# Kernel optimization log

Hardware: AMD Instinct MI355X
Metric: run time of the kernel (lower is better)

Reference implementation:

```python
import jax, jax.numpy as jnp
import numpy as np

B, R, IMG_DIM, TAG_DIM = 256, 36, 2048, 768
BOX_LEN = 15
POS_EMBED = 200
POS_SIZE = 16 * 16 + 1  # 257
EMBED_SIZE = 1024
EPS_NORM = 1e-8
EPS_ATTN = 1e-6


def setup_inputs() -> dict:
    key = jax.random.key(0)
    ks = jax.random.split(key, 8)
    images = jax.random.normal(ks[0], (B, R, IMG_DIM), dtype=jnp.float32)
    images_tag = jax.random.normal(ks[1], (B, R, TAG_DIM), dtype=jnp.float32)
    # boxes: first 15 entries are integer position indices, last 15 are weights
    box_idx = jax.random.randint(ks[2], (B, R, BOX_LEN), 0, POS_SIZE).astype(jnp.float32)
    box_w = jax.random.uniform(ks[3], (B, R, BOX_LEN), dtype=jnp.float32)
    boxes = jnp.concatenate([box_idx, box_w], axis=-1)  # [B,R,30]
    # parameters (xavier-uniform-like for linears, normal for embedding)
    pos_emb = jax.random.normal(ks[4], (POS_SIZE, POS_EMBED), dtype=jnp.float32)
    fan = (IMG_DIM + TAG_DIM) + POS_EMBED
    r1 = np.sqrt(6.0) / np.sqrt(fan)
    attn_W = jax.random.uniform(ks[5], (POS_EMBED, IMG_DIM + TAG_DIM), dtype=jnp.float32, minval=-r1, maxval=r1)
    fc_in = IMG_DIM + POS_EMBED + TAG_DIM
    r2 = np.sqrt(6.0) / np.sqrt(fc_in + EMBED_SIZE)
    fc_W = jax.random.uniform(ks[6], (EMBED_SIZE, fc_in), dtype=jnp.float32, minval=-r2, maxval=r2)
    fc_b = jnp.zeros((EMBED_SIZE,), dtype=jnp.float32)
    return {"images": images, "images_tag": images_tag, "boxes": boxes,
            "pos_emb": pos_emb, "attn_W": attn_W, "fc_W": fc_W, "fc_b": fc_b}


def reference(images, images_tag, boxes, pos_emb, attn_W, fc_W, fc_b):
    half = boxes.shape[2] // 2  # 15
    idx = boxes[..., :half].astype(jnp.int32)        # [B,R,15] position indices
    box_w = boxes[..., half:]                        # [B,R,15] weights
    img_tag = jnp.concatenate([images, images_tag], axis=-1)  # [B,R,2816]
    box_emb = pos_emb[idx]                           # [B,R,15,200]
    # posi_attn (vectorized over batch instead of python loop)
    region = jnp.einsum('brd,ed->bre', img_tag, attn_W)        # [B,R,200]
    scores = jnp.einsum('bre,brke->brk', region, box_emb)      # [B,R,15]
    attn = jax.nn.softmax(jnp.tanh(scores), axis=-1)
    attn = attn * box_w
    attn = attn / (jnp.sum(attn, axis=-1, keepdims=True) + EPS_ATTN)
    box_feat = jnp.einsum('brk,brke->bre', attn, box_emb)      # [B,R,200]
    # original uses .data -> detached attention output
    box_feat = jax.lax.stop_gradient(box_feat)
    image_position = jnp.concatenate([images, box_feat, images_tag], axis=-1)  # [B,R,3016]
    features = jnp.einsum('brd,ed->bre', image_position, fc_W) + fc_b
    norm = jnp.sqrt(jnp.sum(features ** 2, axis=-1, keepdims=True)) + EPS_NORM
    return features / norm
```

## Files before the change

kernel.cpp:

```cpp
#include <hip/hip_runtime.h>


#define M_TOT 9216
#define K1    2816
#define K2    3072
#define ES    1024

typedef __attribute__((ext_vector_type(8))) short bf16x8;
typedef __attribute__((ext_vector_type(4))) float floatx4;

static __device__ __forceinline__ unsigned short f2bf(float f) {
    unsigned int u = __float_as_uint(f);
    u += 0x7fffu + ((u >> 16) & 1u);
    return (unsigned short)(u >> 16);
}

static __device__ __forceinline__ void cvt8(const float* __restrict__ g,
                                            unsigned short* __restrict__ d) {
    const float4 f0 = *(const float4*)g;
    const float4 f1 = *(const float4*)(g + 4);
    uint4 pk;
    pk.x = (unsigned)f2bf(f0.x) | ((unsigned)f2bf(f0.y) << 16);
    pk.y = (unsigned)f2bf(f0.z) | ((unsigned)f2bf(f0.w) << 16);
    pk.z = (unsigned)f2bf(f1.x) | ((unsigned)f2bf(f1.y) << 16);
    pk.w = (unsigned)f2bf(f1.z) | ((unsigned)f2bf(f1.w) << 16);
    *(uint4*)d = pk;
}

static __device__ __forceinline__ void gl16(const void* g, const void* l) {
    __builtin_amdgcn_global_load_lds(
        (const __attribute__((address_space(1))) unsigned int*)g,
        (__attribute__((address_space(3))) unsigned int*)(unsigned int)(unsigned long long)l,
        16, 0, 0);
}

#define NC_ABF (9216 * 352)
#define NC_WF  (1024 * 384)
#define NC_WA  ( 208 * 352)
__global__ __launch_bounds__(256) void k_prep(
    const float* __restrict__ images,
    const float* __restrict__ tag,
    const float* __restrict__ attn_W,
    const float* __restrict__ fc_W,
    unsigned short* __restrict__ Abf,
    unsigned short* __restrict__ Wa,
    unsigned short* __restrict__ Wf)
{
    const int u = blockIdx.x * 256 + threadIdx.x;
    uint4 z; z.x = z.y = z.z = z.w = 0u;
    if (u < NC_ABF) {
        const int m = u / 352;
        const int c = u - m * 352;
        if (c < 256) cvt8(images + (long)m * 2048 + c * 8, Abf + (long)m * K2 + c * 8);
        else         cvt8(tag + (long)m * 768 + (c - 256) * 8,
                          Abf + (long)m * K2 + 2304 + (c - 256) * 8);
    } else if (u < NC_ABF + NC_WF) {
        const int v = u - NC_ABF;
        const int r = v / 384;
        const int dc = (v - r * 384) * 8;
        unsigned short* d = Wf + (long)r * K2 + dc;
        if (dc < 2248)      cvt8(fc_W + (long)r * 3016 + dc, d);
        else if (dc < 2304) *(uint4*)d = z;
        else                cvt8(fc_W + (long)r * 3016 + (dc - 56), d);
    } else if (u < NC_ABF + NC_WF + NC_WA) {
        const int v = u - NC_ABF - NC_WF;
        const int r = v / 352;
        const int c = (v - r * 352) * 8;
        if (r < 200) cvt8(attn_W + (long)r * K1 + c, Wa + (long)r * K1 + c);
        else         *(uint4*)(Wa + (long)r * K1 + c) = z;
    }
}

__global__ __launch_bounds__(256, 4) void k_gemm1_attn(
    const unsigned short* __restrict__ Abf,
    const unsigned short* __restrict__ Wa,
    const float* __restrict__ boxes,
    const float* __restrict__ pos_emb,
    unsigned short* __restrict__ AbfBox)
{
    __shared__ __align__(16) unsigned short lds[14336];
    unsigned short* ldsA = lds;
    unsigned short* ldsB = lds + 1024;
    float* ldsR = (float*)lds;

    const int t = threadIdx.x;
    const int lane = t & 63;
    const int w = t >> 6;
    const int quad = lane >> 4;
    const int ln15 = lane & 15;
    const int x7 = ln15 & 7;
    const int m0 = blockIdx.x * 16;
    const int lrow = lane >> 3;
    const int schunk = (lane & 7) ^ lrow;
    const int nj = (w == 0) ? 4 : 3;

    floatx4 acc[4] = {};

    for (int kt = 0; kt < 44; ++kt) {
        const int kb = kt * 64;
        const int acol = kb + ((kb >= 2048) ? 256 : 0);
#pragma unroll
        for (int i = 0; i < 7; ++i) {
            const int u = w + i * 4;
            if (u < 26) {
                const int r = u * 8 + lrow;
                gl16(Wa + (long)r * K1 + kb + schunk * 8, ldsB + u * 512);
            } else {
                const int r = (u - 26) * 8 + lrow;
                gl16(Abf + (long)(m0 + r) * K2 + acol + schunk * 8,
                     ldsA + (u - 26) * 512);
            }
        }
        __syncthreads();
#pragma unroll
        for (int s = 0; s < 2; ++s) {
            const int g = s * 4 + quad;
            const int co = (g ^ x7) << 3;
            const bf16x8 a = *(const bf16x8*)&ldsA[ln15 * 64 + co];
#pragma unroll
            for (int jj = 0; jj < 4; ++jj) {
                if (jj < nj) {
                    const int j = w + jj * 4;
                    const bf16x8 b = *(const bf16x8*)&ldsB[(j * 16 + ln15) * 64 + co];
                    acc[jj] = __builtin_amdgcn_mfma_f32_16x16x32_bf16(a, b, acc[jj], 0, 0, 0);
                }
            }
        }
        __syncthreads();
    }

#pragma unroll
    for (int jj = 0; jj < 4; ++jj) {
        if (jj < nj) {
            const int j = w + jj * 4;
#pragma unroll
            for (int r = 0; r < 4; ++r)
                ldsR[(quad * 4 + r) * 212 + j * 16 + ln15] = acc[jj][r];
        }
    }
    __syncthreads();

    for (int rr = 0; rr < 4; ++rr) {
        const int ml = w * 4 + rr;
        const int m = m0 + ml;
        float rv[4];
#pragma unroll
        for (int c = 0; c < 4; ++c) {
            const int e = lane + c * 64;
            rv[c] = (e < 200) ? ldsR[ml * 212 + e] : 0.0f;
        }
        const float* bx = boxes + (long)m * 30;
        int idx[15]; float bw[15], sc_[15];
#pragma unroll
        for (int k = 0; k < 15; ++k) {
            int ii = (int)bx[k];
            idx[k] = (ii < 0) ? 0 : (ii > 256 ? 256 : ii);
            bw[k] = bx[15 + k];
        }
#pragma unroll
        for (int k = 0; k < 15; ++k) {
            const float* em = pos_emb + (long)idx[k] * 200;
            float p = 0.0f;
#pragma unroll
            for (int c = 0; c < 4; ++c) {
                const int e = lane + c * 64;
                if (e < 200) p += rv[c] * em[e];
            }
            for (int off = 32; off; off >>= 1) p += __shfl_xor(p, off, 64);
            sc_[k] = p;
        }
        float mx = -1e30f;
#pragma unroll
        for (int k = 0; k < 15; ++k) { sc_[k] = tanhf(sc_[k]); mx = fmaxf(mx, sc_[k]); }
        float Z = 0.0f, den = 0.0f, pk[15];
#pragma unroll
        for (int k = 0; k < 15; ++k) { pk[k] = __expf(sc_[k] - mx); Z += pk[k]; }
#pragma unroll
        for (int k = 0; k < 15; ++k) { pk[k] *= bw[k]; den += pk[k]; }
        den += 1e-6f * Z;
        const float inv = 1.0f / den;
        unsigned short* bo = AbfBox + (long)m * K2 + 2048;
#pragma unroll
        for (int c = 0; c < 4; ++c) {
            const int e = lane + c * 64;
            float o = 0.0f;
            if (e < 200) {
#pragma unroll
                for (int k = 0; k < 15; ++k) o += pk[k] * pos_emb[(long)idx[k] * 200 + e];
                o *= inv;
            }
            bo[e] = f2bf(o);
        }
    }
}

__global__ __launch_bounds__(256, 4) void k_gemm2(
    const unsigned short* __restrict__ Abf,
    const unsigned short* __restrict__ Wf,
    float* __restrict__ dout)
{
    __shared__ __align__(16) unsigned short ldsA[128 * 64];
    __shared__ __align__(16) unsigned short ldsB[128 * 64];
    const int t = threadIdx.x;
    const int lane = t & 63;
    const int w = t >> 6;
    const int quad = lane >> 4;
    const int ln15 = lane & 15;
    const int x7 = ln15 & 7;
    const int m0 = blockIdx.x * 128;
    const int n0 = blockIdx.y * 128;
    const int lrow = lane >> 3;
    const int schunk = (lane & 7) ^ lrow;
    const int wm = (w & 1) * 64;
    const int wn = (w >> 1) * 64;

    floatx4 acc[4][4] = {};

    for (int kt = 0; kt < 48; ++kt) {
        const int kb = kt * 64;
#pragma unroll
        for (int i = 0; i < 4; ++i) {
            const int u = w * 4 + i;
            const int r = u * 8 + lrow;
            gl16(Abf + (long)(m0 + r) * K2 + kb + schunk * 8, ldsA + u * 512);
            gl16(Wf  + (long)(n0 + r) * K2 + kb + schunk * 8, ldsB + u * 512);
        }
        __syncthreads();
#pragma unroll
        for (int s = 0; s < 2; ++s) {
            const int g = s * 4 + quad;
            const int co = (g ^ x7) << 3;
            bf16x8 a[4], b[4];
#pragma unroll
            for (int i = 0; i < 4; ++i)
                a[i] = *(const bf16x8*)&ldsA[(wm + i * 16 + ln15) * 64 + co];
#pragma unroll
            for (int j = 0; j < 4; ++j)
                b[j] = *(const bf16x8*)&ldsB[(wn + j * 16 + ln15) * 64 + co];
#pragma unroll
            for (int i = 0; i < 4; ++i)
#pragma unroll
                for (int j = 0; j < 4; ++j)
                    acc[i][j] = __builtin_amdgcn_mfma_f32_16x16x32_bf16(a[i], b[j], acc[i][j], 0, 0, 0);
        }
        __syncthreads();
    }
#pragma unroll
    for (int i = 0; i < 4; ++i)
#pragma unroll
        for (int j = 0; j < 4; ++j) {
            const int row = m0 + wm + i * 16 + quad * 4;
            const int col = n0 + wn + j * 16 + ln15;
#pragma unroll
            for (int r = 0; r < 4; ++r)
                dout[(long)(row + r) * ES + col] = acc[i][j][r];
        }
}

__global__ __launch_bounds__(256) void k_norm(
    float* __restrict__ dout,
    const float* __restrict__ bias)
{
    __shared__ float red[4];
    const int m = blockIdx.x;
    const int t = threadIdx.x;
    float* f = dout + (long)m * ES + t * 4;
    float4 v = *(const float4*)f;
    const float4 bs = *(const float4*)(bias + t * 4);
    v.x += bs.x; v.y += bs.y; v.z += bs.z; v.w += bs.w;
    float ss = v.x * v.x + v.y * v.y + v.z * v.z + v.w * v.w;
    for (int off = 32; off; off >>= 1) ss += __shfl_xor(ss, off, 64);
    if ((t & 63) == 0) red[t >> 6] = ss;
    __syncthreads();
    const float total = red[0] + red[1] + red[2] + red[3];
    const float inv = 1.0f / (sqrtf(total) + 1e-8f);
    float4 o;
    o.x = v.x * inv; o.y = v.y * inv; o.z = v.z * inv; o.w = v.w * inv;
    *(float4*)f = o;
}

extern "C" void kernel_launch(void* const* d_in, const int* in_sizes, int n_in,
                              void* d_out, int out_size, void* d_ws, size_t ws_size,
                              hipStream_t stream) {
    const float* images  = (const float*)d_in[0];
    const float* tag     = (const float*)d_in[1];
    const float* boxes   = (const float*)d_in[2];
    const float* pos_emb = (const float*)d_in[3];
    const float* attn_W  = (const float*)d_in[4];
    const float* fc_W    = (const float*)d_in[5];
    const float* fc_b    = (const float*)d_in[6];
    float* out = (float*)d_out;

    unsigned short* Abf = (unsigned short*)d_ws;
    unsigned short* Wf  = Abf + (size_t)M_TOT * K2;
    unsigned short* Wa  = Wf  + (size_t)ES * K2;

    const int prep_blocks = (NC_ABF + NC_WF + NC_WA + 255) / 256;
    k_prep      <<<prep_blocks, 256, 0, stream>>>(images, tag, attn_W, fc_W, Abf, Wa, Wf);
    k_gemm1_attn<<<576, 256, 0, stream>>>(Abf, Wa, boxes, pos_emb, Abf);
    k_gemm2     <<<dim3(72, 8), 256, 0, stream>>>(Abf, Wf, out);
    k_norm      <<<M_TOT, 256, 0, stream>>>(out, fc_b);
}
```

Baseline: 316.0 us.

## Fuse activation bf16 conversion into gemm1, split-K gemm1, separate attention kernel

The bf16 conversion of images and tags now happens inside the first GEMM, which loads the fp32 activations, packs them into LDS and also writes the bf16 copy that the second GEMM reuses. This drops a separate full pass over the activations. The first GEMM is split in K across two blocks per row tile to double the block count, and it writes fp32 partial results to a workspace. A new attention kernel sums the two partials and runs the softmax and box pooling with one wave per row. The second GEMM's grid is transposed so blocks that share an M tile run adjacently, which should improve reuse of A in cache. The cost is an extra kernel launch and a round trip of the partials through global memory.

```diff
diff --git a/kernel.cpp b/kernel.cpp
--- a/kernel.cpp
+++ b/kernel.cpp
@@ -5,6 +5,7 @@
 #define K1    2816
 #define K2    3072
 #define ES    1024
+#define REGN  (9216L * 208)
 
 typedef __attribute__((ext_vector_type(8))) short bf16x8;
 typedef __attribute__((ext_vector_type(4))) float floatx4;
@@ -15,16 +16,18 @@
     return (unsigned short)(u >> 16);
 }
 
-static __device__ __forceinline__ void cvt8(const float* __restrict__ g,
-                                            unsigned short* __restrict__ d) {
-    const float4 f0 = *(const float4*)g;
-    const float4 f1 = *(const float4*)(g + 4);
+static __device__ __forceinline__ uint4 pack8(const float4 f0, const float4 f1) {
     uint4 pk;
     pk.x = (unsigned)f2bf(f0.x) | ((unsigned)f2bf(f0.y) << 16);
     pk.y = (unsigned)f2bf(f0.z) | ((unsigned)f2bf(f0.w) << 16);
     pk.z = (unsigned)f2bf(f1.x) | ((unsigned)f2bf(f1.y) << 16);
     pk.w = (unsigned)f2bf(f1.z) | ((unsigned)f2bf(f1.w) << 16);
-    *(uint4*)d = pk;
+    return pk;
+}
+
+static __device__ __forceinline__ void cvt8(const float* __restrict__ g,
+                                            unsigned short* __restrict__ d) {
+    *(uint4*)d = pack8(*(const float4*)g, *(const float4*)(g + 4));
 }
 
 static __device__ __forceinline__ void gl16(const void* g, const void* l) {
@@ -34,36 +37,25 @@
         16, 0, 0);
 }
 
-#define NC_ABF (9216 * 352)
 #define NC_WF  (1024 * 384)
 #define NC_WA  ( 208 * 352)
-__global__ __launch_bounds__(256) void k_prep(
-    const float* __restrict__ images,
-    const float* __restrict__ tag,
+__global__ __launch_bounds__(256) void k_prep_w(
     const float* __restrict__ attn_W,
     const float* __restrict__ fc_W,
-    unsigned short* __restrict__ Abf,
     unsigned short* __restrict__ Wa,
     unsigned short* __restrict__ Wf)
 {
     const int u = blockIdx.x * 256 + threadIdx.x;
     uint4 z; z.x = z.y = z.z = z.w = 0u;
-    if (u < NC_ABF) {
-        const int m = u / 352;
-        const int c = u - m * 352;
-        if (c < 256) cvt8(images + (long)m * 2048 + c * 8, Abf + (long)m * K2 + c * 8);
-        else         cvt8(tag + (long)m * 768 + (c - 256) * 8,
-                          Abf + (long)m * K2 + 2304 + (c - 256) * 8);
-    } else if (u < NC_ABF + NC_WF) {
-        const int v = u - NC_ABF;
-        const int r = v / 384;
-        const int dc = (v - r * 384) * 8;
+    if (u < NC_WF) {
+        const int r = u / 384;
+        const int dc = (u - r * 384) * 8;
         unsigned short* d = Wf + (long)r * K2 + dc;
         if (dc < 2248)      cvt8(fc_W + (long)r * 3016 + dc, d);
         else if (dc < 2304) *(uint4*)d = z;
         else                cvt8(fc_W + (long)r * 3016 + (dc - 56), d);
-    } else if (u < NC_ABF + NC_WF + NC_WA) {
-        const int v = u - NC_ABF - NC_WF;
+    } else if (u < NC_WF + NC_WA) {
+        const int v = u - NC_WF;
         const int r = v / 352;
         const int c = (v - r * 352) * 8;
         if (r < 200) cvt8(attn_W + (long)r * K1 + c, Wa + (long)r * K1 + c);
@@ -71,17 +63,16 @@
     }
 }
 
-__global__ __launch_bounds__(256, 4) void k_gemm1_attn(
-    const unsigned short* __restrict__ Abf,
+__global__ __launch_bounds__(256, 5) void k_gemm1(
+    const float* __restrict__ images,
+    const float* __restrict__ tag,
     const unsigned short* __restrict__ Wa,
-    const float* __restrict__ boxes,
-    const float* __restrict__ pos_emb,
-    unsigned short* __restrict__ AbfBox)
+    unsigned short* __restrict__ Abf,
+    float* __restrict__ regP)
 {
     __shared__ __align__(16) unsigned short lds[14336];
     unsigned short* ldsA = lds;
     unsigned short* ldsB = lds + 1024;
-    float* ldsR = (float*)lds;
 
     const int t = threadIdx.x;
     const int lane = t & 63;
@@ -89,27 +80,51 @@
     const int quad = lane >> 4;
     const int ln15 = lane & 15;
     const int x7 = ln15 & 7;
-    const int m0 = blockIdx.x * 16;
+    const int bid = blockIdx.x;
+    const int m0 = (bid >> 1) * 16;
+    const int kh = bid & 1;
+    const int kbase = kh * 1408;
     const int lrow = lane >> 3;
     const int schunk = (lane & 7) ^ lrow;
     const int nj = (w == 0) ? 4 : 3;
 
+    const bool stA = (t < 128);
+    const int sr = t >> 3;
+    const int sgl = t & 7;
+    const int aslot = sr * 64 + ((sgl ^ (sr & 7)) << 3);
+
     floatx4 acc[4] = {};
-
-    for (int kt = 0; kt < 44; ++kt) {
-        const int kb = kt * 64;
-        const int acol = kb + ((kb >= 2048) ? 256 : 0);
+    float4 v0, v1;
+
+    if (stA) {
+        const float* src = (kbase < 2048)
+            ? images + (long)(m0 + sr) * 2048 + kbase + sgl * 8
+            : tag + (long)(m0 + sr) * 768 + (kbase - 2048) + sgl * 8;
+        v0 = *(const float4*)src;
+        v1 = *(const float4*)(src + 4);
+    }
+
+    for (int kt = 0; kt < 22; ++kt) {
+        const int kb = kbase + kt * 64;
+        if (stA) {
+            const uint4 pk = pack8(v0, v1);
+            *(uint4*)&ldsA[aslot] = pk;
+            const int acol = kb + ((kb >= 2048) ? 256 : 0);
+            *(uint4*)(Abf + (long)(m0 + sr) * K2 + acol + sgl * 8) = pk;
+            if (kt < 21) {
+                const int kn = kb + 64;
+                const float* src = (kn < 2048)
+                    ? images + (long)(m0 + sr) * 2048 + kn + sgl * 8
+                    : tag + (long)(m0 + sr) * 768 + (kn - 2048) + sgl * 8;
+                v0 = *(const float4*)src;
+                v1 = *(const float4*)(src + 4);
+            }
+        }
 #pragma unroll
         for (int i = 0; i < 7; ++i) {
             const int u = w + i * 4;
-            if (u < 26) {
-                const int r = u * 8 + lrow;
-                gl16(Wa + (long)r * K1 + kb + schunk * 8, ldsB + u * 512);
-            } else {
-                const int r = (u - 26) * 8 + lrow;
-                gl16(Abf + (long)(m0 + r) * K2 + acol + schunk * 8,
-                     ldsA + (u - 26) * 512);
-            }
+            if (u < 26)
+                gl16(Wa + (long)(u * 8 + lrow) * K1 + kb + schunk * 8, ldsB + u * 512);
         }
         __syncthreads();
 #pragma unroll
@@ -129,68 +144,78 @@
         __syncthreads();
     }
 
+    float* rp = regP + (long)kh * REGN;
 #pragma unroll
     for (int jj = 0; jj < 4; ++jj) {
         if (jj < nj) {
             const int j = w + jj * 4;
 #pragma unroll
             for (int r = 0; r < 4; ++r)
-                ldsR[(quad * 4 + r) * 212 + j * 16 + ln15] = acc[jj][r];
-        }
-    }
-    __syncthreads();
-
-    for (int rr = 0; rr < 4; ++rr) {
-        const int ml = w * 4 + rr;
-        const int m = m0 + ml;
-        float rv[4];
+                rp[(long)(m0 + quad * 4 + r) * 208 + j * 16 + ln15] = acc[jj][r];
+        }
+    }
+}
+
+__global__ __launch_bounds__(256, 4) void k_attn(
+    const float* __restrict__ regP,
+    const float* __restrict__ boxes,
+    const float* __restrict__ pos_emb,
+    unsigned short* __restrict__ Abf)
+{
+    const int t = threadIdx.x;
+    const int lane = t & 63;
+    const int w = t >> 6;
+    const int m = blockIdx.x * 4 + w;
+
+    const float* r0 = regP + (long)m * 208;
+    const float* r1 = r0 + REGN;
+    float rv[4];
+#pragma unroll
+    for (int c = 0; c < 4; ++c) {
+        const int e = lane + c * 64;
+        rv[c] = (e < 200) ? (r0[e] + r1[e]) : 0.0f;
+    }
+    const float* bx = boxes + (long)m * 30;
+    int idx[15]; float bw[15], sc_[15];
+#pragma unroll
+    for (int k = 0; k < 15; ++k) {
+        int ii = (int)bx[k];
+        idx[k] = (ii < 0) ? 0 : (ii > 256 ? 256 : ii);
+        bw[k] = bx[15 + k];
+    }
+#pragma unroll
+    for (int k = 0; k < 15; ++k) {
+        const float* em = pos_emb + (long)idx[k] * 200;
+        float p = 0.0f;
 #pragma unroll
         for (int c = 0; c < 4; ++c) {
             const int e = lane + c * 64;
-            rv[c] = (e < 200) ? ldsR[ml * 212 + e] : 0.0f;
-        }
-        const float* bx = boxes + (long)m * 30;
-        int idx[15]; float bw[15], sc_[15];
-#pragma unroll
-        for (int k = 0; k < 15; ++k) {
-            int ii = (int)bx[k];
-            idx[k] = (ii < 0) ? 0 : (ii > 256 ? 256 : ii);
-            bw[k] = bx[15 + k];
-        }
-#pragma unroll
-        for (int k = 0; k < 15; ++k) {
-            const float* em = pos_emb + (long)idx[k] * 200;
-            float p = 0.0f;
-#pragma unroll
-            for (int c = 0; c < 4; ++c) {
-                const int e = lane + c * 64;
-                if (e < 200) p += rv[c] * em[e];
-            }
-            for (int off = 32; off; off >>= 1) p += __shfl_xor(p, off, 64);
-            sc_[k] = p;
-        }
-        float mx = -1e30f;
-#pragma unroll
-        for (int k = 0; k < 15; ++k) { sc_[k] = tanhf(sc_[k]); mx = fmaxf(mx, sc_[k]); }
-        float Z = 0.0f, den = 0.0f, pk[15];
-#pragma unroll
-        for (int k = 0; k < 15; ++k) { pk[k] = __expf(sc_[k] - mx); Z += pk[k]; }
-#pragma unroll
-        for (int k = 0; k < 15; ++k) { pk[k] *= bw[k]; den += pk[k]; }
-        den += 1e-6f * Z;
-        const float inv = 1.0f / den;
-        unsigned short* bo = AbfBox + (long)m * K2 + 2048;
-#pragma unroll
-        for (int c = 0; c < 4; ++c) {
-            const int e = lane + c * 64;
-            float o = 0.0f;
-            if (e < 200) {
-#pragma unroll
-                for (int k = 0; k < 15; ++k) o += pk[k] * pos_emb[(long)idx[k] * 200 + e];
-                o *= inv;
-            }
-            bo[e] = f2bf(o);
-        }
+            if (e < 200) p += rv[c] * em[e];
+        }
+        for (int off = 32; off; off >>= 1) p += __shfl_xor(p, off, 64);
+        sc_[k] = p;
+    }
+    float mx = -1e30f;
+#pragma unroll
+    for (int k = 0; k < 15; ++k) { sc_[k] = tanhf(sc_[k]); mx = fmaxf(mx, sc_[k]); }
+    float Z = 0.0f, den = 0.0f, pk[15];
+#pragma unroll
+    for (int k = 0; k < 15; ++k) { pk[k] = __expf(sc_[k] - mx); Z += pk[k]; }
+#pragma unroll
+    for (int k = 0; k < 15; ++k) { pk[k] *= bw[k]; den += pk[k]; }
+    den += 1e-6f * Z;
+    const float inv = 1.0f / den;
+    unsigned short* bo = Abf + (long)m * K2 + 2048;
+#pragma unroll
+    for (int c = 0; c < 4; ++c) {
+        const int e = lane + c * 64;
+        float o = 0.0f;
+        if (e < 200) {
+#pragma unroll
+            for (int k = 0; k < 15; ++k) o += pk[k] * pos_emb[(long)idx[k] * 200 + e];
+            o *= inv;
+        }
+        bo[e] = f2bf(o);
     }
 }
 
@@ -207,8 +232,8 @@
     const int quad = lane >> 4;
     const int ln15 = lane & 15;
     const int x7 = ln15 & 7;
-    const int m0 = blockIdx.x * 128;
-    const int n0 = blockIdx.y * 128;
+    const int n0 = blockIdx.x * 128;
+    const int m0 = blockIdx.y * 128;
     const int lrow = lane >> 3;
     const int schunk = (lane & 7) ^ lrow;
     const int wm = (w & 1) * 64;
@@ -294,10 +319,11 @@
     unsigned short* Abf = (unsigned short*)d_ws;
     unsigned short* Wf  = Abf + (size_t)M_TOT * K2;
     unsigned short* Wa  = Wf  + (size_t)ES * K2;
-
-    const int prep_blocks = (NC_ABF + NC_WF + NC_WA + 255) / 256;
-    k_prep      <<<prep_blocks, 256, 0, stream>>>(images, tag, attn_W, fc_W, Abf, Wa, Wf);
-    k_gemm1_attn<<<576, 256, 0, stream>>>(Abf, Wa, boxes, pos_emb, Abf);
-    k_gemm2     <<<dim3(72, 8), 256, 0, stream>>>(Abf, Wf, out);
-    k_norm      <<<M_TOT, 256, 0, stream>>>(out, fc_b);
-}
+    float* regP = (float*)(Wa + (size_t)208 * K1);
+
+    k_prep_w<<<1822, 256, 0, stream>>>(attn_W, fc_W, Wa, Wf);
+    k_gemm1 <<<1152, 256, 0, stream>>>(images, tag, Wa, Abf, regP);
+    k_attn  <<<2304, 256, 0, stream>>>(regP, boxes, pos_emb, Abf);
+    k_gemm2 <<<dim3(8, 72), 256, 0, stream>>>(Abf, Wf, out);
+    k_norm  <<<M_TOT, 256, 0, stream>>>(out, fc_b);
+}
```

Result: slower. 328.0 us (+3.8%).
